# Optimization experiments

Hardware: AMD Instinct MI355X
Metric: run time of the kernel (lower is better)

The kernel has to match this reference:

```python
import jax, jax.numpy as jnp
import numpy as np

THRESHOLD = 0.05
STRIDE = (1, 1)
PADDING = ((1, 1), (1, 1))


def ternary_quantize(w, threshold=THRESHOLD):
    # w -> {-1, 0, +1}; zero where |w| <= threshold
    mask = (jnp.abs(w) > threshold).astype(w.dtype)
    return jnp.sign(w) * mask


def setup_inputs() -> dict:
    key = jax.random.key(0)
    k1, k2 = jax.random.split(key)
    B, Cin, H, W = 32, 256, 56, 56
    Cout, kH, kW = 256, 3, 3
    fan_in = Cin * kH * kW
    std = np.sqrt(2.0 / fan_in) * 2.0
    x = jax.random.normal(k1, (B, Cin, H, W), dtype=jnp.float32)
    weight = jax.random.normal(k2, (Cout, Cin, kH, kW), dtype=jnp.float32) * std
    bias = jnp.zeros((Cout,), dtype=jnp.float32)
    return {"x": x, "weight": weight, "bias": bias}


def reference(x, weight, bias):
    w_t = ternary_quantize(weight, THRESHOLD)
    out = jax.lax.conv_general_dilated(
        x, w_t,
        window_strides=STRIDE,
        padding=PADDING,
        dimension_numbers=("NCHW", "OIHW", "NCHW"),
    )
    return out + bias[None, :, None, None]
```

## Files before the change

### kernel.cpp

```cpp
#include <hip/hip_runtime.h>

#define CIN   256
#define COUT  256
#define HH    56
#define WW    56
#define BATCH 32
#define KTOT  2304
#define HP    58
#define WP    58
#define NPIX  (BATCH*HH*WW)
#define HWSZ  (HH*WW)

typedef __bf16 bf16x8 __attribute__((ext_vector_type(8)));
typedef float  f32x4  __attribute__((ext_vector_type(4)));

#define AS1 __attribute__((address_space(1)))
#define AS3 __attribute__((address_space(3)))

__device__ __forceinline__ unsigned short f2bf(float f) {
  union { float f; unsigned int u; } v; v.f = f;
  unsigned int u = v.u;
  u += 0x7fffu + ((u >> 16) & 1u);
  return (unsigned short)(u >> 16);
}

__device__ __forceinline__ void async16(const void* g, void* l) {
  __builtin_amdgcn_global_load_lds((const AS1 unsigned int*)g,
                                   (AS3 unsigned int*)l, 16, 0, 0);
}

__global__ __launch_bounds__(256) void quant_w(const float* __restrict__ w,
                                               unsigned short* __restrict__ wr) {
  int tid = blockIdx.x * 256 + threadIdx.x;
  if (tid >= COUT * KTOT) return;
  int co  = tid / KTOT;
  int rem = tid - co * KTOT;
  int tap = rem >> 8;
  int ci  = rem & 255;
  int kh  = tap / 3;
  int kw  = tap - kh * 3;
  float v = w[((co * CIN + ci) * 3 + kh) * 3 + kw];
  float q = (fabsf(v) > 0.05f) ? ((v > 0.f) ? 1.f : -1.f) : 0.f;
  wr[tid] = f2bf(q);
}

__global__ __launch_bounds__(256) void pad_nhwc(const float* __restrict__ x,
                                                unsigned short* __restrict__ xp) {
  const int nhp = blockIdx.x;
  const int n   = nhp / HP;
  const int hp  = nhp - n * HP;
  const int ci0 = blockIdx.y * 64;
  const int t   = threadIdx.x;
  const size_t obase = (size_t)nhp * (WP * 256);

  __shared__ float tile[64 * 56];
  const bool hborder = (hp == 0) || (hp == HP - 1);

  if (!hborder) {
    const int h = hp - 1;
    #pragma unroll
    for (int it = 0; it < 14; ++it) {
      int linear = it * 256 + t;
      int cil  = linear / 56;
      int wcol = linear - cil * 56;
      tile[cil * 56 + wcol] =
          x[(((size_t)(n * CIN + ci0 + cil)) * HH + h) * WW + wcol];
    }
  }
  __syncthreads();

  #pragma unroll
  for (int it = 0; it < 2; ++it) {
    int linear = it * 256 + t;
    if (linear < 464) {
      int wp = linear >> 3;
      int g  = linear & 7;
      unsigned int pk[4] = {0u, 0u, 0u, 0u};
      if (!hborder && wp != 0 && wp != WP - 1) {
        #pragma unroll
        for (int j = 0; j < 4; ++j) {
          unsigned int lo = f2bf(tile[(g * 8 + 2 * j) * 56 + (wp - 1)]);
          unsigned int hi = f2bf(tile[(g * 8 + 2 * j + 1) * 56 + (wp - 1)]);
          pk[j] = lo | (hi << 16);
        }
      }
      uint4 v; v.x = pk[0]; v.y = pk[1]; v.z = pk[2]; v.w = pk[3];
      *(uint4*)(xp + obase + (size_t)wp * 256 + ci0 + g * 8) = v;
    }
  }
}

__global__ __launch_bounds__(256, 2) void conv_gemm(
    const unsigned short* __restrict__ Wr,
    const unsigned short* __restrict__ Xp,
    const float* __restrict__ bias,
    float* __restrict__ out) {
  __shared__ __align__(16) unsigned short a_tile[128 * 32];
  __shared__ __align__(16) unsigned short b_tile[128 * 32];

  const int t    = threadIdx.x;
  const int lane = t & 63;
  const int wv   = t >> 6;
  const int wm   = wv >> 1;
  const int wn   = wv & 1;
  const int l15  = lane & 15;
  const int quad = lane >> 4;

  const int co0 = blockIdx.y * 128;
  const int p0  = blockIdx.x * 128;

  const int srow = t >> 2;
  const int scol = t & 3;

  const size_t aIdx0 = (size_t)(co0 + srow) * KTOT + scol * 8;
  const size_t aIdx1 = aIdx0 + (size_t)64 * KTOT;

  const int pA = p0 + srow;
  const int pB = pA + 64;
  const int nA = pA / HWSZ;  const int hwA = pA - nA * HWSZ;
  const int hA = hwA / WW;   const int wA  = hwA - hA * WW;
  const int nB = pB / HWSZ;  const int hwB = pB - nB * HWSZ;
  const int hB = hwB / WW;   const int wB  = hwB - hB * WW;
  const size_t bIdx0 = ((size_t)((nA * HP + hA) * WP + wA)) * 256 + scol * 8;
  const size_t bIdx1 = ((size_t)((nB * HP + hB) * WP + wB)) * 256 + scol * 8;

  f32x4 acc[4][4];
  #pragma unroll
  for (int i = 0; i < 4; ++i)
    #pragma unroll
    for (int j = 0; j < 4; ++j)
      acc[i][j] = (f32x4){0.f, 0.f, 0.f, 0.f};

  for (int kk = 0; kk < KTOT / 32; ++kk) {
    const int tap   = kk >> 3;
    const int cio   = (kk & 7) << 5;
    const int kh    = tap / 3;
    const int kw    = tap - kh * 3;
    const int koffW = kk << 5;
    const int koffX = (kh * WP + kw) * 256 + cio;

    __syncthreads();
    async16(Wr + koffW + aIdx0, a_tile + t * 8);
    async16(Wr + koffW + aIdx1, a_tile + 2048 + t * 8);
    async16(Xp + koffX + bIdx0, b_tile + t * 8);
    async16(Xp + koffX + bIdx1, b_tile + 2048 + t * 8);
    __syncthreads();

    bf16x8 af[4], bfr[4];
    #pragma unroll
    for (int mt = 0; mt < 4; ++mt)
      af[mt] = *(const bf16x8*)(a_tile + ((wm * 64 + mt * 16 + l15) * 32 + quad * 8));
    #pragma unroll
    for (int nt = 0; nt < 4; ++nt)
      bfr[nt] = *(const bf16x8*)(b_tile + ((wn * 64 + nt * 16 + l15) * 32 + quad * 8));

    #pragma unroll
    for (int mt = 0; mt < 4; ++mt)
      #pragma unroll
      for (int nt = 0; nt < 4; ++nt)
        acc[mt][nt] = __builtin_amdgcn_mfma_f32_16x16x32_bf16(
            af[mt], bfr[nt], acc[mt][nt], 0, 0, 0);
  }

  float bv[4][4];
  #pragma unroll
  for (int mt = 0; mt < 4; ++mt)
    #pragma unroll
    for (int r = 0; r < 4; ++r)
      bv[mt][r] = bias[co0 + wm * 64 + mt * 16 + quad * 4 + r];

  #pragma unroll
  for (int nt = 0; nt < 4; ++nt) {
    const int p  = p0 + wn * 64 + nt * 16 + l15;
    const int np = p / HWSZ;
    const int hw = p - np * HWSZ;
    const size_t obase = (size_t)np * (COUT * HWSZ) + hw;
    #pragma unroll
    for (int mt = 0; mt < 4; ++mt) {
      const int co = co0 + wm * 64 + mt * 16 + quad * 4;
      #pragma unroll
      for (int r = 0; r < 4; ++r)
        out[obase + (size_t)(co + r) * HWSZ] = acc[mt][nt][r] + bv[mt][r];
    }
  }
}

extern "C" void kernel_launch(void* const* d_in, const int* in_sizes, int n_in,
                              void* d_out, int out_size, void* d_ws, size_t ws_size,
                              hipStream_t stream) {
  const float* x    = (const float*)d_in[0];
  const float* w    = (const float*)d_in[1];
  const float* bias = (const float*)d_in[2];
  float* out        = (float*)d_out;

  unsigned short* xp = (unsigned short*)d_ws;
  unsigned short* wr = (unsigned short*)((char*)d_ws + 55115776);

  quant_w<<<dim3((COUT * KTOT) / 256), dim3(256), 0, stream>>>(w, wr);
  pad_nhwc<<<dim3(BATCH * HP, 4), dim3(256), 0, stream>>>(x, xp);
  conv_gemm<<<dim3(NPIX / 128, 2), dim3(256), 0, stream>>>(wr, xp, bias, out);
}
```

Before: 358.2 us.

## Double-buffer conv GEMM LDS tiles, remap blocks per XCD, vectorize pad loads

The conv GEMM now keeps two LDS stages and issues the async global-to-LDS loads for the next K slice while MFMAs run on the current one, replacing the two barriers per iteration with one. The grid is flattened to 1D and remapped so consecutive logical tiles, including both output-channel halves of a pixel tile, land on the same XCD, which is meant to improve L2 reuse of the input tile. The pad kernel reads input rows as float4 instead of scalar floats. Doubling LDS per block may affect occupancy, and correctness depends on the async LDS writes being complete by the time of the single barrier.

```diff
diff --git a/kernel.cpp b/kernel.cpp
--- a/kernel.cpp
+++ b/kernel.cpp
@@ -53,18 +53,20 @@
   const int t   = threadIdx.x;
   const size_t obase = (size_t)nhp * (WP * 256);
 
-  __shared__ float tile[64 * 56];
+  __shared__ __align__(16) float tile[64 * 56];
   const bool hborder = (hp == 0) || (hp == HP - 1);
 
   if (!hborder) {
     const int h = hp - 1;
     #pragma unroll
-    for (int it = 0; it < 14; ++it) {
+    for (int it = 0; it < 4; ++it) {
       int linear = it * 256 + t;
-      int cil  = linear / 56;
-      int wcol = linear - cil * 56;
-      tile[cil * 56 + wcol] =
-          x[(((size_t)(n * CIN + ci0 + cil)) * HH + h) * WW + wcol];
+      if (linear < 896) {
+        int cil = linear / 14;
+        int w4  = linear - cil * 14;
+        *(float4*)&tile[cil * 56 + w4 * 4] =
+            *(const float4*)&x[(((size_t)(n * CIN + ci0 + cil)) * HH + h) * WW + w4 * 4];
+      }
     }
   }
   __syncthreads();
@@ -95,8 +97,8 @@
     const unsigned short* __restrict__ Xp,
     const float* __restrict__ bias,
     float* __restrict__ out) {
-  __shared__ __align__(16) unsigned short a_tile[128 * 32];
-  __shared__ __align__(16) unsigned short b_tile[128 * 32];
+  __shared__ __align__(16) unsigned short a_tile[2][128 * 32];
+  __shared__ __align__(16) unsigned short b_tile[2][128 * 32];
 
   const int t    = threadIdx.x;
   const int lane = t & 63;
@@ -106,8 +108,15 @@
   const int l15  = lane & 15;
   const int quad = lane >> 4;
 
-  const int co0 = blockIdx.y * 128;
-  const int p0  = blockIdx.x * 128;
+  const int f   = blockIdx.x;
+  const int xcd = f & 7;
+  const int pos = f >> 3;
+  const int nf  = xcd * 196 + pos;
+  const int cob = nf & 1;
+  const int pb  = nf >> 1;
+
+  const int co0 = cob * 128;
+  const int p0  = pb * 128;
 
   const int srow = t >> 2;
   const int scol = t & 3;
@@ -124,35 +133,43 @@
   const size_t bIdx0 = ((size_t)((nA * HP + hA) * WP + wA)) * 256 + scol * 8;
   const size_t bIdx1 = ((size_t)((nB * HP + hB) * WP + wB)) * 256 + scol * 8;
 
-  f32x4 acc[4][4];
-  #pragma unroll
-  for (int i = 0; i < 4; ++i)
-    #pragma unroll
-    for (int j = 0; j < 4; ++j)
-      acc[i][j] = (f32x4){0.f, 0.f, 0.f, 0.f};
-
-  for (int kk = 0; kk < KTOT / 32; ++kk) {
+  auto stage = [&](int kk, int s) {
     const int tap   = kk >> 3;
     const int cio   = (kk & 7) << 5;
     const int kh    = tap / 3;
     const int kw    = tap - kh * 3;
     const int koffW = kk << 5;
     const int koffX = (kh * WP + kw) * 256 + cio;
-
-    __syncthreads();
-    async16(Wr + koffW + aIdx0, a_tile + t * 8);
-    async16(Wr + koffW + aIdx1, a_tile + 2048 + t * 8);
-    async16(Xp + koffX + bIdx0, b_tile + t * 8);
-    async16(Xp + koffX + bIdx1, b_tile + 2048 + t * 8);
-    __syncthreads();
+    async16(Wr + koffW + aIdx0, &a_tile[s][0] + t * 8);
+    async16(Wr + koffW + aIdx1, &a_tile[s][0] + 2048 + t * 8);
+    async16(Xp + koffX + bIdx0, &b_tile[s][0] + t * 8);
+    async16(Xp + koffX + bIdx1, &b_tile[s][0] + 2048 + t * 8);
+  };
+
+  f32x4 acc[4][4];
+  #pragma unroll
+  for (int i = 0; i < 4; ++i)
+    #pragma unroll
+    for (int j = 0; j < 4; ++j)
+      acc[i][j] = (f32x4){0.f, 0.f, 0.f, 0.f};
+
+  stage(0, 0);
+  __syncthreads();
+
+  for (int kk = 0; kk < KTOT / 32; ++kk) {
+    const int cur = kk & 1;
+    if (kk < KTOT / 32 - 1)
+      stage(kk + 1, cur ^ 1);
 
     bf16x8 af[4], bfr[4];
     #pragma unroll
     for (int mt = 0; mt < 4; ++mt)
-      af[mt] = *(const bf16x8*)(a_tile + ((wm * 64 + mt * 16 + l15) * 32 + quad * 8));
+      af[mt] = *(const bf16x8*)(&a_tile[cur][0] +
+                                ((wm * 64 + mt * 16 + l15) * 32 + quad * 8));
     #pragma unroll
     for (int nt = 0; nt < 4; ++nt)
-      bfr[nt] = *(const bf16x8*)(b_tile + ((wn * 64 + nt * 16 + l15) * 32 + quad * 8));
+      bfr[nt] = *(const bf16x8*)(&b_tile[cur][0] +
+                                 ((wn * 64 + nt * 16 + l15) * 32 + quad * 8));
 
     #pragma unroll
     for (int mt = 0; mt < 4; ++mt)
@@ -160,6 +177,8 @@
       for (int nt = 0; nt < 4; ++nt)
         acc[mt][nt] = __builtin_amdgcn_mfma_f32_16x16x32_bf16(
             af[mt], bfr[nt], acc[mt][nt], 0, 0, 0);
+
+    __syncthreads();
   }
 
   float bv[4][4];
@@ -198,5 +217,5 @@
 
   quant_w<<<dim3((COUT * KTOT) / 256), dim3(256), 0, stream>>>(w, wr);
   pad_nhwc<<<dim3(BATCH * HP, 4), dim3(256), 0, stream>>>(x, xp);
-  conv_gemm<<<dim3(NPIX / 128, 2), dim3(256), 0, stream>>>(wr, xp, bias, out);
-}
+  conv_gemm<<<dim3(NPIX / 128 * 2), dim3(256), 0, stream>>>(wr, xp, bias, out);
+}
```

Result: faster. 337.8 us (-5.7%).
